# Performance work log

Measured on AMD Instinct MI355X. Metric: run time of the kernel, lower is better.

## Reference

```python
import jax, jax.numpy as jnp
import numpy as np

N_NODES, N_EDGES = 50000, 800000
N_IN, E_IN, N_OUT, E_OUT = 64, 32, 64, 32


def _xavier(key, fan_in, fan_out):
    std = (2.0 / (fan_in + fan_out)) ** 0.5
    return jax.random.normal(key, (fan_in, fan_out), dtype=jnp.float32) * std


def setup_inputs() -> dict:
    key = jax.random.key(0)
    ks = jax.random.split(key, 10)
    return {
        "feat": jax.random.normal(ks[0], (N_NODES, N_IN), dtype=jnp.float32),
        "edge_feat": jax.random.normal(ks[1], (N_EDGES, E_IN), dtype=jnp.float32),
        "w_msg": _xavier(ks[2], N_IN + E_IN, N_OUT),
        "b_msg": jnp.zeros((N_OUT,), dtype=jnp.float32),
        "w_node": _xavier(ks[3], N_IN + N_OUT, N_OUT),
        "b_node": jnp.zeros((N_OUT,), dtype=jnp.float32),
        "w_edge": _xavier(ks[4], N_IN + N_OUT + E_IN, E_OUT),
        "b_edge": jnp.zeros((E_OUT,), dtype=jnp.float32),
        "src_idx": jax.random.randint(ks[5], (N_EDGES,), 0, N_NODES, dtype=jnp.int32),
        "dst_idx": jax.random.randint(ks[6], (N_EDGES,), 0, N_NODES, dtype=jnp.int32),
    }


def reference(feat, edge_feat, w_msg, b_msg, w_node, b_node, w_edge, b_edge, src_idx, dst_idx):
    n_nodes = feat.shape[0]
    # --- message: gather src + edge, linear, tanh --- [E, n_out]
    src_h = feat[src_idx]
    m = jnp.tanh(jnp.concatenate([src_h, edge_feat], axis=1) @ w_msg + b_msg)
    # --- scatter-mean into destination nodes --- [N, n_out]
    sums = jax.ops.segment_sum(m, dst_idx, num_segments=n_nodes)
    cnt = jax.ops.segment_sum(jnp.ones((m.shape[0], 1), m.dtype), dst_idx, num_segments=n_nodes)
    neigh = sums / jnp.maximum(cnt, 1.0)
    # --- node update: cat([neigh, h]) -> linear -> tanh (dropout = identity in eval) ---
    h = jnp.tanh(jnp.concatenate([neigh, feat], axis=1) @ w_node + b_node)
    # --- edge update: cat([src h, dst neigh(updated), edge h]) -> linear -> tanh ---
    e = jnp.tanh(jnp.concatenate([src_h, h[dst_idx], edge_feat], axis=1) @ w_edge + b_edge)
    return h, e
```

## Files before the change

### kernel.cpp

```cpp
#include <hip/hip_runtime.h>

#define NNODES 50000
#define NEDGES 800000
#define NPAD   50176
#define NTILE_E (NEDGES / 16)
#define NTILE_N (NNODES / 16)

typedef __attribute__((ext_vector_type(8))) short bf16x8;
typedef __attribute__((ext_vector_type(4))) float f32x4;

union ABu { bf16x8 v; uint4 u; };

__device__ __forceinline__ float fast_tanh(float x) {
    float e = __expf(2.0f * x);
    return 1.0f - 2.0f * __builtin_amdgcn_rcpf(e + 1.0f);
}

__device__ __forceinline__ unsigned pk_rne(float x, float y) {
    unsigned a = __float_as_uint(x), b = __float_as_uint(y);
    a = (a + 0x7fffu + ((a >> 16) & 1u)) >> 16;
    b = (b + 0x7fffu + ((b >> 16) & 1u)) >> 16;
    return a | (b << 16);
}
__device__ __forceinline__ unsigned pk_tr(float a, float b) {
    return __builtin_amdgcn_perm(__float_as_uint(b), __float_as_uint(a), 0x07060302);
}
__device__ __forceinline__ float bf16_lo(unsigned u) { return __uint_as_float(u << 16); }
__device__ __forceinline__ float bf16_hi(unsigned u) { return __uint_as_float(u & 0xffff0000u); }

__device__ __forceinline__ ABu make_afrag(const float* p) {
    float4 a = ((const float4*)p)[0];
    float4 b = ((const float4*)p)[1];
    ABu r;
    r.u.x = pk_tr(a.x, a.y); r.u.y = pk_tr(a.z, a.w);
    r.u.z = pk_tr(b.x, b.y); r.u.w = pk_tr(b.z, b.w);
    return r;
}

template <int LDN>
__device__ __forceinline__ ABu make_bfrag_u(const unsigned* wp) {
    ABu r;
    r.u.x = wp[0 * LDN]; r.u.y = wp[1 * LDN];
    r.u.z = wp[2 * LDN]; r.u.w = wp[3 * LDN];
    return r;
}

template <int KH, int N>
__device__ __forceinline__ void stage_w(const float* __restrict__ w, unsigned* wl_u) {
    for (int i = threadIdx.x; i < KH * N; i += 256) {
        const int kp = i / N, n = i % N;
        wl_u[i] = pk_rne(w[(2 * kp) * N + n], w[(2 * kp + 1) * N + n]);
    }
}

#define MFMA(a, b, c) __builtin_amdgcn_mfma_f32_16x16x32_bf16((a).v, (b).v, (c), 0, 0, 0)

__global__ __launch_bounds__(256) void hist_kernel(const int* __restrict__ dst_idx,
                                                   int* __restrict__ cnt,
                                                   int* __restrict__ rank) {
    const int base = (blockIdx.x * 256 + threadIdx.x) * 4;
    if (base + 4 <= NEDGES) {
        int4 d = *(const int4*)(dst_idx + base);
        int4 r;
        r.x = atomicAdd(&cnt[d.x], 1);
        r.y = atomicAdd(&cnt[d.y], 1);
        r.z = atomicAdd(&cnt[d.z], 1);
        r.w = atomicAdd(&cnt[d.w], 1);
        *(int4*)(rank + base) = r;
    } else {
        for (int i = base; i < NEDGES; ++i) rank[i] = atomicAdd(&cnt[dst_idx[i]], 1);
    }
}

__global__ __launch_bounds__(256) void scan1(const int* __restrict__ cnt,
                                             int* __restrict__ off,
                                             int* __restrict__ btot) {
    __shared__ int s[256];
    const int tid = threadIdx.x;
    const int g = blockIdx.x * 256 + tid;
    const int own = cnt[g];
    s[tid] = own;
    __syncthreads();
    for (int o = 1; o < 256; o <<= 1) {
        int v = (tid >= o) ? s[tid - o] : 0;
        __syncthreads();
        s[tid] += v;
        __syncthreads();
    }
    off[g] = s[tid] - own;
    if (tid == 255) btot[blockIdx.x] = s[255];
}

__global__ __launch_bounds__(256) void scan2(int* __restrict__ btot) {
    __shared__ int s[256];
    const int tid = threadIdx.x;
    const int own = btot[tid];
    s[tid] = own;
    __syncthreads();
    for (int o = 1; o < 256; o <<= 1) {
        int v = (tid >= o) ? s[tid - o] : 0;
        __syncthreads();
        s[tid] += v;
        __syncthreads();
    }
    btot[tid] = s[tid] - own;
}

__global__ __launch_bounds__(256) void scan3(int* __restrict__ off,
                                             const int* __restrict__ btot) {
    const int g = blockIdx.x * 256 + threadIdx.x;
    off[g] += btot[blockIdx.x];
}

struct MsgBuf { ABu a0, a1, a2; int4 rows; };

__device__ __forceinline__ void msg_load(
    int t, int col, int quad,
    const float* __restrict__ feat, const float* __restrict__ edge_feat,
    const int* __restrict__ src_idx, const int* __restrict__ dst_idx,
    const int* __restrict__ off, const int* __restrict__ rank, MsgBuf& b) {
    const int e0 = t << 4;
    const int e = e0 + col;
    const int src = src_idx[e];
    const int4 d4 = *(const int4*)(dst_idx + e0 + (quad << 2));
    const int4 r4 = *(const int4*)(rank + e0 + (quad << 2));
    b.rows.x = off[d4.x] + r4.x;
    b.rows.y = off[d4.y] + r4.y;
    b.rows.z = off[d4.z] + r4.z;
    b.rows.w = off[d4.w] + r4.w;
    b.a0 = make_afrag(feat + (size_t)src * 64 + (quad << 3));
    b.a1 = make_afrag(feat + (size_t)src * 64 + 32 + (quad << 3));
    b.a2 = make_afrag(edge_feat + (size_t)e * 32 + (quad << 3));
}

__device__ __forceinline__ void msg_comp(
    int col, const ABu (&bf)[3][4], const float (&bias)[4],
    const MsgBuf& b, unsigned* __restrict__ m_out) {
    f32x4 acc[4];
#pragma unroll
    for (int nt = 0; nt < 4; ++nt)
        acc[nt] = (f32x4){bias[nt], bias[nt], bias[nt], bias[nt]};
#pragma unroll
    for (int nt = 0; nt < 4; ++nt) {
        acc[nt] = MFMA(b.a0, bf[0][nt], acc[nt]);
        acc[nt] = MFMA(b.a1, bf[1][nt], acc[nt]);
        acc[nt] = MFMA(b.a2, bf[2][nt], acc[nt]);
    }
    const int rw[4] = {b.rows.x, b.rows.y, b.rows.z, b.rows.w};
#pragma unroll
    for (int i = 0; i < 4; ++i) {
        uint2 o;
        o.x = pk_rne(fast_tanh(acc[0][i]), fast_tanh(acc[1][i]));
        o.y = pk_rne(fast_tanh(acc[2][i]), fast_tanh(acc[3][i]));
        *(uint2*)(m_out + (size_t)rw[i] * 32 + (col << 1)) = o;
    }
}

__global__ __launch_bounds__(256) void msg_kernel(
    const float* __restrict__ feat, const float* __restrict__ edge_feat,
    const float* __restrict__ w_msg, const float* __restrict__ b_msg,
    const int* __restrict__ src_idx, const int* __restrict__ dst_idx,
    const int* __restrict__ off, const int* __restrict__ rank,
    unsigned* __restrict__ m_out) {
    __shared__ __align__(16) unsigned wl[48 * 64];
    stage_w<48, 64>(w_msg, wl);
    __syncthreads();

    const int lane = threadIdx.x & 63, wave = threadIdx.x >> 6;
    const int col = lane & 15, quad = lane >> 4;

    ABu bf[3][4];
#pragma unroll
    for (int kc = 0; kc < 3; ++kc)
#pragma unroll
        for (int nt = 0; nt < 4; ++nt)
            bf[kc][nt] = make_bfrag_u<64>(&wl[(kc * 16 + (quad << 2)) * 64 + nt * 16 + col]);

    float bias[4];
#pragma unroll
    for (int nt = 0; nt < 4; ++nt) bias[nt] = b_msg[nt * 16 + col];

    const int nw = gridDim.x << 2;
    int t = (blockIdx.x << 2) + wave;
    if (t >= NTILE_E) return;
    MsgBuf A, B;
    msg_load(t, col, quad, feat, edge_feat, src_idx, dst_idx, off, rank, A);
    for (;;) {
        const int t2 = t + nw;
        if (t2 < NTILE_E)
            msg_load(t2, col, quad, feat, edge_feat, src_idx, dst_idx, off, rank, B);
        msg_comp(col, bf, bias, A, m_out);
        if (t2 >= NTILE_E) return;
        const int t3 = t2 + nw;
        if (t3 < NTILE_E)
            msg_load(t3, col, quad, feat, edge_feat, src_idx, dst_idx, off, rank, A);
        msg_comp(col, bf, bias, B, m_out);
        if (t3 >= NTILE_E) return;
        t = t3;
    }
}

__global__ __launch_bounds__(256) void gather_kernel(
    const unsigned* __restrict__ m,
    const int* __restrict__ off , const int* __restrict__ cnt,
    float* __restrict__ neigh) {
    const int wave = threadIdx.x >> 6;
    const int lane = threadIdx.x & 63;
    const int n = blockIdx.x * 4 + wave;
    if (n >= NNODES) return;
    const int c = cnt[n];
    const int o = off[n];
    const int q = lane & 7;
    const int g = lane >> 3;

    float s[8];
#pragma unroll
    for (int j = 0; j < 8; ++j) s[j] = 0.f;
    for (int r = g; r < c; r += 8) {
        const uint4 u = *(const uint4*)(m + (size_t)(o + r) * 32 + (q << 2));
        s[0] += bf16_lo(u.x); s[1] += bf16_hi(u.x);
        s[2] += bf16_lo(u.y); s[3] += bf16_hi(u.y);
        s[4] += bf16_lo(u.z); s[5] += bf16_hi(u.z);
        s[6] += bf16_lo(u.w); s[7] += bf16_hi(u.w);
    }
#pragma unroll
    for (int j = 0; j < 8; ++j) {
        s[j] += __shfl_xor(s[j], 8);
        s[j] += __shfl_xor(s[j], 16);
        s[j] += __shfl_xor(s[j], 32);
    }
    if (g == 0) {
        const float inv = __builtin_amdgcn_rcpf((float)max(c, 1));
        float4 o0 = {s[0] * inv, s[1] * inv, s[2] * inv, s[3] * inv};
        float4 o1 = {s[4] * inv, s[5] * inv, s[6] * inv, s[7] * inv};
        float* dst = neigh + (size_t)n * 64 + (q << 3);
        ((float4*)dst)[0] = o0;
        ((float4*)dst)[1] = o1;
    }
}

__device__ __forceinline__ int mapk(int ks) {
    return ks < 64 ? ((ks >> 2) + ((ks >> 1) & 1) * 32 + (ks & 1) * 16) : ks;
}

__global__ __launch_bounds__(256) void node_update(
    const float* __restrict__ feat,
    const float* __restrict__ w_node, const float* __restrict__ b_node,
    float* __restrict__ h) {
    __shared__ __align__(16) float wl[128 * 64];
    for (int i = threadIdx.x; i < 128 * 64; i += 256) wl[i] = w_node[i];
    __syncthreads();

    const int lane = threadIdx.x & 63, wave = threadIdx.x >> 6;
    const int col = lane & 15, quad = lane >> 4;

    ABu bf[4][4];
#pragma unroll
    for (int kc = 0; kc < 4; ++kc)
#pragma unroll
        for (int nt = 0; nt < 4; ++nt) {
            unsigned p[4];
#pragma unroll
            for (int jj = 0; jj < 4; ++jj) {
                const int k0 = kc * 32 + quad * 8 + jj * 2;
                p[jj] = pk_rne(wl[mapk(k0) * 64 + nt * 16 + col],
                               wl[mapk(k0 + 1) * 64 + nt * 16 + col]);
            }
            bf[kc][nt].u = (uint4){p[0], p[1], p[2], p[3]};
        }

    float bias[4];
#pragma unroll
    for (int nt = 0; nt < 4; ++nt) bias[nt] = b_node[nt * 16 + col];

    const int nw = gridDim.x << 2;
    for (int t = (blockIdx.x << 2) + wave; t < NTILE_N; t += nw) {
        const int n0 = t << 4;
        const int n = n0 + col;
        ABu a0 = make_afrag(h + (size_t)n * 64 + quad * 8);
        ABu a1 = make_afrag(h + (size_t)n * 64 + 32 + quad * 8);
        ABu a2 = make_afrag(feat + (size_t)n * 64 + quad * 8);
        ABu a3 = make_afrag(feat + (size_t)n * 64 + 32 + quad * 8);

        f32x4 acc[4];
#pragma unroll
        for (int nt = 0; nt < 4; ++nt)
            acc[nt] = (f32x4){bias[nt], bias[nt], bias[nt], bias[nt]};
#pragma unroll
        for (int nt = 0; nt < 4; ++nt) {
            acc[nt] = MFMA(a0, bf[0][nt], acc[nt]);
            acc[nt] = MFMA(a1, bf[1][nt], acc[nt]);
            acc[nt] = MFMA(a2, bf[2][nt], acc[nt]);
            acc[nt] = MFMA(a3, bf[3][nt], acc[nt]);
        }
#pragma unroll
        for (int i = 0; i < 4; ++i) {
            const int nr = n0 + quad * 4 + i;
#pragma unroll
            for (int nt = 0; nt < 4; ++nt)
                h[(size_t)nr * 64 + nt * 16 + col] = fast_tanh(acc[nt][i]);
        }
    }
}

struct EBuf { ABu a0, a1, a2, a3, a4; };

__device__ __forceinline__ void edge_load(
    int t, int col, int quad,
    const float* __restrict__ feat, const float* __restrict__ edge_feat,
    const float* __restrict__ h,
    const int* __restrict__ src_idx, const int* __restrict__ dst_idx, EBuf& b) {
    const int e = (t << 4) + col;
    const int src = src_idx[e];
    const int dst = dst_idx[e];
    b.a0 = make_afrag(feat + (size_t)src * 64 + (quad << 3));
    b.a1 = make_afrag(feat + (size_t)src * 64 + 32 + (quad << 3));
    b.a2 = make_afrag(h + (size_t)dst * 64 + (quad << 3));
    b.a3 = make_afrag(h + (size_t)dst * 64 + 32 + (quad << 3));
    b.a4 = make_afrag(edge_feat + (size_t)e * 32 + (quad << 3));
}

__device__ __forceinline__ void edge_comp(
    int t, int col, int quad, const ABu (&bf)[5][2], const float (&bias)[2],
    const EBuf& b, float* __restrict__ e_out) {
    f32x4 acc[2];
#pragma unroll
    for (int nt = 0; nt < 2; ++nt)
        acc[nt] = (f32x4){bias[nt], bias[nt], bias[nt], bias[nt]};
#pragma unroll
    for (int nt = 0; nt < 2; ++nt) {
        acc[nt] = MFMA(b.a0, bf[0][nt], acc[nt]);
        acc[nt] = MFMA(b.a1, bf[1][nt], acc[nt]);
        acc[nt] = MFMA(b.a2, bf[2][nt], acc[nt]);
        acc[nt] = MFMA(b.a3, bf[3][nt], acc[nt]);
        acc[nt] = MFMA(b.a4, bf[4][nt], acc[nt]);
    }
    const int e0 = t << 4;
#pragma unroll
    for (int i = 0; i < 4; ++i) {
        const int er = e0 + quad * 4 + i;
        e_out[(size_t)er * 32 + col] = fast_tanh(acc[0][i]);
        e_out[(size_t)er * 32 + 16 + col] = fast_tanh(acc[1][i]);
    }
}

__global__ __launch_bounds__(256) void edge_update(
    const float* __restrict__ feat, const float* __restrict__ edge_feat,
    const float* __restrict__ h,
    const float* __restrict__ w_edge, const float* __restrict__ b_edge,
    const int* __restrict__ src_idx, const int* __restrict__ dst_idx,
    float* __restrict__ e_out) {
    __shared__ __align__(16) unsigned wl[80 * 32];
    stage_w<80, 32>(w_edge, wl);
    __syncthreads();

    const int lane = threadIdx.x & 63, wave = threadIdx.x >> 6;
    const int col = lane & 15, quad = lane >> 4;

    ABu bf[5][2];
#pragma unroll
    for (int kc = 0; kc < 5; ++kc)
#pragma unroll
        for (int nt = 0; nt < 2; ++nt)
            bf[kc][nt] = make_bfrag_u<32>(&wl[(kc * 16 + (quad << 2)) * 32 + nt * 16 + col]);

    float bias[2];
#pragma unroll
    for (int nt = 0; nt < 2; ++nt) bias[nt] = b_edge[nt * 16 + col];

    const int nw = gridDim.x << 2;
    int t = (blockIdx.x << 2) + wave;
    if (t >= NTILE_E) return;
    EBuf A, B;
    edge_load(t, col, quad, feat, edge_feat, h, src_idx, dst_idx, A);
    for (;;) {
        const int t2 = t + nw;
        if (t2 < NTILE_E)
            edge_load(t2, col, quad, feat, edge_feat, h, src_idx, dst_idx, B);
        edge_comp(t, col, quad, bf, bias, A, e_out);
        if (t2 >= NTILE_E) return;
        const int t3 = t2 + nw;
        if (t3 < NTILE_E)
            edge_load(t3, col, quad, feat, edge_feat, h, src_idx, dst_idx, A);
        edge_comp(t2, col, quad, bf, bias, B, e_out);
        if (t3 >= NTILE_E) return;
        t = t3;
    }
}

extern "C" void kernel_launch(void* const* d_in, const int* in_sizes, int n_in,
                              void* d_out, int out_size, void* d_ws, size_t ws_size,
                              hipStream_t stream) {
    const float* feat      = (const float*)d_in[0];
    const float* edge_feat = (const float*)d_in[1];
    const float* w_msg     = (const float*)d_in[2];
    const float* b_msg     = (const float*)d_in[3];
    const float* w_node    = (const float*)d_in[4];
    const float* b_node    = (const float*)d_in[5];
    const float* w_edge    = (const float*)d_in[6];
    const float* b_edge    = (const float*)d_in[7];
    const int*   src_idx   = (const int*)d_in[8];
    const int*   dst_idx   = (const int*)d_in[9];

    float* h = (float*)d_out;
    float* e = (float*)d_out + (size_t)NNODES * 64;
    unsigned* m = (unsigned*)e;

    int* cnt  = (int*)d_ws;
    int* off  = cnt + NPAD;
    int* btot = off + NPAD;
    int* rank = btot + 256;

    hipMemsetAsync(cnt, 0, NPAD * sizeof(int), stream);
    hipMemsetAsync(btot, 0, 256 * sizeof(int), stream);

    hist_kernel<<<(NEDGES / 4 + 255) / 256, 256, 0, stream>>>(dst_idx, cnt, rank);
    scan1<<<NPAD / 256, 256, 0, stream>>>(cnt, off, btot);
    scan2<<<1, 256, 0, stream>>>(btot);
    scan3<<<NPAD / 256, 256, 0, stream>>>(off, btot);
    msg_kernel<<<1536, 256, 0, stream>>>(feat, edge_feat, w_msg, b_msg,
                                         src_idx, dst_idx, off, rank, m);
    gather_kernel<<<NNODES / 4, 256, 0, stream>>>(m, off, cnt, h);
    node_update<<<512, 256, 0, stream>>>(feat, w_node, b_node, h);
    edge_update<<<1280, 256, 0, stream>>>(feat, edge_feat, h, w_edge,
                                          b_edge, src_idx, dst_idx, e);
}
```

Measured before the change: 414.6 us.

## Precompute per-node projections before gathering in message and edge kernels

The message and edge linear layers are split by linearity. The feat and h parts are projected once per node (50K rows) by a new proj_kernel, and the edge kernels then gather the smaller projected rows instead of the raw 64-wide features. This cuts per-edge MFMA work and per-edge gather width: the edge kernel gathers 32+32 floats instead of 128, and the message kernel gathers 64 projected floats. It adds three small projection launches and workspace buffers. The message projection reuses the h output buffer as scratch before the gather kernel writes h.

```diff
diff --git a/kernel.cpp b/kernel.cpp
--- a/kernel.cpp
+++ b/kernel.cpp
@@ -112,89 +112,134 @@
     off[g] += btot[blockIdx.x];
 }
 
-struct MsgBuf { ABu a0, a1, a2; int4 rows; };
+template <int KC, int NT>
+__global__ __launch_bounds__(256) void proj_kernel(
+    const float* __restrict__ in, const float* __restrict__ w,
+    const float* __restrict__ bias, float* __restrict__ out) {
+    constexpr int N = NT * 16;
+    constexpr int K = KC * 32;
+    __shared__ __align__(16) unsigned wl[(K / 2) * N];
+    stage_w<K / 2, N>(w, wl);
+    __syncthreads();
+
+    const int lane = threadIdx.x & 63, wave = threadIdx.x >> 6;
+    const int col = lane & 15, quad = lane >> 4;
+
+    ABu bf[KC][NT];
+#pragma unroll
+    for (int kc = 0; kc < KC; ++kc)
+#pragma unroll
+        for (int nt = 0; nt < NT; ++nt)
+            bf[kc][nt] = make_bfrag_u<N>(&wl[(kc * 16 + (quad << 2)) * N + nt * 16 + col]);
+
+    float bi[NT];
+#pragma unroll
+    for (int nt = 0; nt < NT; ++nt) bi[nt] = bias ? bias[nt * 16 + col] : 0.f;
+
+    const int nw = gridDim.x << 2;
+    for (int t = (blockIdx.x << 2) + wave; t < NTILE_N; t += nw) {
+        const int n0 = t << 4;
+        const int n = n0 + col;
+        ABu a[KC];
+#pragma unroll
+        for (int kc = 0; kc < KC; ++kc)
+            a[kc] = make_afrag(in + (size_t)n * K + kc * 32 + (quad << 3));
+
+        f32x4 acc[NT];
+#pragma unroll
+        for (int nt = 0; nt < NT; ++nt)
+            acc[nt] = (f32x4){bi[nt], bi[nt], bi[nt], bi[nt]};
+#pragma unroll
+        for (int nt = 0; nt < NT; ++nt)
+#pragma unroll
+            for (int kc = 0; kc < KC; ++kc)
+                acc[nt] = MFMA(a[kc], bf[kc][nt], acc[nt]);
+
+#pragma unroll
+        for (int i = 0; i < 4; ++i) {
+            const int nr = n0 + (quad << 2) + i;
+            if (NT == 4) {
+                float4 o = {acc[0][i], acc[1][i], acc[2][i], acc[3][i]};
+                *(float4*)(out + (size_t)nr * 64 + (col << 2)) = o;
+            } else {
+                float2 o = {acc[0][i], acc[1][i]};
+                *(float2*)(out + (size_t)nr * 32 + (col << 1)) = o;
+            }
+        }
+    }
+}
+
+struct MsgBuf { ABu a2; float4 f4[4]; int4 rows; };
 
 __device__ __forceinline__ void msg_load(
     int t, int col, int quad,
-    const float* __restrict__ feat, const float* __restrict__ edge_feat,
+    const float* __restrict__ edge_feat, const float* __restrict__ projm,
     const int* __restrict__ src_idx, const int* __restrict__ dst_idx,
     const int* __restrict__ off, const int* __restrict__ rank, MsgBuf& b) {
     const int e0 = t << 4;
-    const int e = e0 + col;
-    const int src = src_idx[e];
+    const int4 s4 = *(const int4*)(src_idx + e0 + (quad << 2));
     const int4 d4 = *(const int4*)(dst_idx + e0 + (quad << 2));
     const int4 r4 = *(const int4*)(rank + e0 + (quad << 2));
     b.rows.x = off[d4.x] + r4.x;
     b.rows.y = off[d4.y] + r4.y;
     b.rows.z = off[d4.z] + r4.z;
     b.rows.w = off[d4.w] + r4.w;
-    b.a0 = make_afrag(feat + (size_t)src * 64 + (quad << 3));
-    b.a1 = make_afrag(feat + (size_t)src * 64 + 32 + (quad << 3));
-    b.a2 = make_afrag(edge_feat + (size_t)e * 32 + (quad << 3));
+    b.a2 = make_afrag(edge_feat + (size_t)(e0 + col) * 32 + (quad << 3));
+    b.f4[0] = *(const float4*)(projm + (size_t)s4.x * 64 + (col << 2));
+    b.f4[1] = *(const float4*)(projm + (size_t)s4.y * 64 + (col << 2));
+    b.f4[2] = *(const float4*)(projm + (size_t)s4.z * 64 + (col << 2));
+    b.f4[3] = *(const float4*)(projm + (size_t)s4.w * 64 + (col << 2));
 }
 
 __device__ __forceinline__ void msg_comp(
-    int col, const ABu (&bf)[3][4], const float (&bias)[4],
-    const MsgBuf& b, unsigned* __restrict__ m_out) {
+    int col, const ABu (&bf)[4], const MsgBuf& b, unsigned* __restrict__ m_out) {
     f32x4 acc[4];
 #pragma unroll
-    for (int nt = 0; nt < 4; ++nt)
-        acc[nt] = (f32x4){bias[nt], bias[nt], bias[nt], bias[nt]};
-#pragma unroll
-    for (int nt = 0; nt < 4; ++nt) {
-        acc[nt] = MFMA(b.a0, bf[0][nt], acc[nt]);
-        acc[nt] = MFMA(b.a1, bf[1][nt], acc[nt]);
-        acc[nt] = MFMA(b.a2, bf[2][nt], acc[nt]);
-    }
+    for (int nt = 0; nt < 4; ++nt) acc[nt] = (f32x4){0.f, 0.f, 0.f, 0.f};
+#pragma unroll
+    for (int nt = 0; nt < 4; ++nt) acc[nt] = MFMA(b.a2, bf[nt], acc[nt]);
     const int rw[4] = {b.rows.x, b.rows.y, b.rows.z, b.rows.w};
 #pragma unroll
     for (int i = 0; i < 4; ++i) {
         uint2 o;
-        o.x = pk_rne(fast_tanh(acc[0][i]), fast_tanh(acc[1][i]));
-        o.y = pk_rne(fast_tanh(acc[2][i]), fast_tanh(acc[3][i]));
+        o.x = pk_rne(fast_tanh(acc[0][i] + b.f4[i].x), fast_tanh(acc[1][i] + b.f4[i].y));
+        o.y = pk_rne(fast_tanh(acc[2][i] + b.f4[i].z), fast_tanh(acc[3][i] + b.f4[i].w));
         *(uint2*)(m_out + (size_t)rw[i] * 32 + (col << 1)) = o;
     }
 }
 
 __global__ __launch_bounds__(256) void msg_kernel(
-    const float* __restrict__ feat, const float* __restrict__ edge_feat,
-    const float* __restrict__ w_msg, const float* __restrict__ b_msg,
+    const float* __restrict__ edge_feat, const float* __restrict__ w_bot,
     const int* __restrict__ src_idx, const int* __restrict__ dst_idx,
     const int* __restrict__ off, const int* __restrict__ rank,
-    unsigned* __restrict__ m_out) {
-    __shared__ __align__(16) unsigned wl[48 * 64];
-    stage_w<48, 64>(w_msg, wl);
+    const float* __restrict__ projm, unsigned* __restrict__ m_out) {
+    __shared__ __align__(16) unsigned wl[16 * 64];
+    stage_w<16, 64>(w_bot, wl);
     __syncthreads();
 
     const int lane = threadIdx.x & 63, wave = threadIdx.x >> 6;
     const int col = lane & 15, quad = lane >> 4;
 
-    ABu bf[3][4];
-#pragma unroll
-    for (int kc = 0; kc < 3; ++kc)
-#pragma unroll
-        for (int nt = 0; nt < 4; ++nt)
-            bf[kc][nt] = make_bfrag_u<64>(&wl[(kc * 16 + (quad << 2)) * 64 + nt * 16 + col]);
-
-    float bias[4];
-#pragma unroll
-    for (int nt = 0; nt < 4; ++nt) bias[nt] = b_msg[nt * 16 + col];
+    ABu bf[4];
+#pragma unroll
+    for (int nt = 0; nt < 4; ++nt)
+        bf[nt] = make_bfrag_u<64>(&wl[(quad << 2) * 64 + nt * 16 + col]);
 
     const int nw = gridDim.x << 2;
     int t = (blockIdx.x << 2) + wave;
     if (t >= NTILE_E) return;
     MsgBuf A, B;
-    msg_load(t, col, quad, feat, edge_feat, src_idx, dst_idx, off, rank, A);
+    msg_load(t, col, quad, edge_feat, projm, src_idx, dst_idx, off, rank, A);
     for (;;) {
         const int t2 = t + nw;
         if (t2 < NTILE_E)
-            msg_load(t2, col, quad, feat, edge_feat, src_idx, dst_idx, off, rank, B);
-        msg_comp(col, bf, bias, A, m_out);
+            msg_load(t2, col, quad, edge_feat, projm, src_idx, dst_idx, off, rank, B);
+        msg_comp(col, bf, A, m_out);
         if (t2 >= NTILE_E) return;
         const int t3 = t2 + nw;
         if (t3 < NTILE_E)
-            msg_load(t3, col, quad, feat, edge_feat, src_idx, dst_idx, off, rank, A);
-        msg_comp(col, bf, bias, B, m_out);
+            msg_load(t3, col, quad, edge_feat, projm, src_idx, dst_idx, off, rank, A);
+        msg_comp(col, bf, B, m_out);
         if (t3 >= NTILE_E) return;
         t = t3;
     }
@@ -303,86 +348,76 @@
     }
 }
 
-struct EBuf { ABu a0, a1, a2, a3, a4; };
+struct EBuf { ABu a4; float2 g1[4]; float2 g2[4]; };
 
 __device__ __forceinline__ void edge_load(
     int t, int col, int quad,
-    const float* __restrict__ feat, const float* __restrict__ edge_feat,
-    const float* __restrict__ h,
+    const float* __restrict__ edge_feat,
+    const float* __restrict__ p1, const float* __restrict__ p2,
     const int* __restrict__ src_idx, const int* __restrict__ dst_idx, EBuf& b) {
-    const int e = (t << 4) + col;
-    const int src = src_idx[e];
-    const int dst = dst_idx[e];
-    b.a0 = make_afrag(feat + (size_t)src * 64 + (quad << 3));
-    b.a1 = make_afrag(feat + (size_t)src * 64 + 32 + (quad << 3));
-    b.a2 = make_afrag(h + (size_t)dst * 64 + (quad << 3));
-    b.a3 = make_afrag(h + (size_t)dst * 64 + 32 + (quad << 3));
-    b.a4 = make_afrag(edge_feat + (size_t)e * 32 + (quad << 3));
+    const int e0 = t << 4;
+    const int4 s4 = *(const int4*)(src_idx + e0 + (quad << 2));
+    const int4 d4 = *(const int4*)(dst_idx + e0 + (quad << 2));
+    b.a4 = make_afrag(edge_feat + (size_t)(e0 + col) * 32 + (quad << 3));
+    b.g1[0] = *(const float2*)(p1 + (size_t)s4.x * 32 + (col << 1));
+    b.g1[1] = *(const float2*)(p1 + (size_t)s4.y * 32 + (col << 1));
+    b.g1[2] = *(const float2*)(p1 + (size_t)s4.z * 32 + (col << 1));
+    b.g1[3] = *(const float2*)(p1 + (size_t)s4.w * 32 + (col << 1));
+    b.g2[0] = *(const float2*)(p2 + (size_t)d4.x * 32 + (col << 1));
+    b.g2[1] = *(const float2*)(p2 + (size_t)d4.y * 32 + (col << 1));
+    b.g2[2] = *(const float2*)(p2 + (size_t)d4.z * 32 + (col << 1));
+    b.g2[3] = *(const float2*)(p2 + (size_t)d4.w * 32 + (col << 1));
 }
 
 __device__ __forceinline__ void edge_comp(
-    int t, int col, int quad, const ABu (&bf)[5][2], const float (&bias)[2],
+    int t, int col, int quad, const ABu (&bf)[2],
     const EBuf& b, float* __restrict__ e_out) {
     f32x4 acc[2];
 #pragma unroll
-    for (int nt = 0; nt < 2; ++nt)
-        acc[nt] = (f32x4){bias[nt], bias[nt], bias[nt], bias[nt]};
-#pragma unroll
-    for (int nt = 0; nt < 2; ++nt) {
-        acc[nt] = MFMA(b.a0, bf[0][nt], acc[nt]);
-        acc[nt] = MFMA(b.a1, bf[1][nt], acc[nt]);
-        acc[nt] = MFMA(b.a2, bf[2][nt], acc[nt]);
-        acc[nt] = MFMA(b.a3, bf[3][nt], acc[nt]);
-        acc[nt] = MFMA(b.a4, bf[4][nt], acc[nt]);
-    }
+    for (int nt = 0; nt < 2; ++nt) acc[nt] = (f32x4){0.f, 0.f, 0.f, 0.f};
+#pragma unroll
+    for (int nt = 0; nt < 2; ++nt) acc[nt] = MFMA(b.a4, bf[nt], acc[nt]);
     const int e0 = t << 4;
 #pragma unroll
     for (int i = 0; i < 4; ++i) {
-        const int er = e0 + quad * 4 + i;
-        e_out[(size_t)er * 32 + col] = fast_tanh(acc[0][i]);
-        e_out[(size_t)er * 32 + 16 + col] = fast_tanh(acc[1][i]);
+        const int er = e0 + (quad << 2) + i;
+        e_out[(size_t)er * 32 + col] = fast_tanh(acc[0][i] + b.g1[i].x + b.g2[i].x);
+        e_out[(size_t)er * 32 + 16 + col] = fast_tanh(acc[1][i] + b.g1[i].y + b.g2[i].y);
     }
 }
 
 __global__ __launch_bounds__(256) void edge_update(
-    const float* __restrict__ feat, const float* __restrict__ edge_feat,
-    const float* __restrict__ h,
-    const float* __restrict__ w_edge, const float* __restrict__ b_edge,
+    const float* __restrict__ edge_feat, const float* __restrict__ w3,
+    const float* __restrict__ p1, const float* __restrict__ p2,
     const int* __restrict__ src_idx, const int* __restrict__ dst_idx,
     float* __restrict__ e_out) {
-    __shared__ __align__(16) unsigned wl[80 * 32];
-    stage_w<80, 32>(w_edge, wl);
+    __shared__ __align__(16) unsigned wl[16 * 32];
+    stage_w<16, 32>(w3, wl);
     __syncthreads();
 
     const int lane = threadIdx.x & 63, wave = threadIdx.x >> 6;
     const int col = lane & 15, quad = lane >> 4;
 
-    ABu bf[5][2];
-#pragma unroll
-    for (int kc = 0; kc < 5; ++kc)
-#pragma unroll
-        for (int nt = 0; nt < 2; ++nt)
-            bf[kc][nt] = make_bfrag_u<32>(&wl[(kc * 16 + (quad << 2)) * 32 + nt * 16 + col]);
-
-    float bias[2];
-#pragma unroll
-    for (int nt = 0; nt < 2; ++nt) bias[nt] = b_edge[nt * 16 + col];
+    ABu bf[2];
+#pragma unroll
+    for (int nt = 0; nt < 2; ++nt)
+        bf[nt] = make_bfrag_u<32>(&wl[(quad << 2) * 32 + nt * 16 + col]);
 
     const int nw = gridDim.x << 2;
     int t = (blockIdx.x << 2) + wave;
     if (t >= NTILE_E) return;
     EBuf A, B;
-    edge_load(t, col, quad, feat, edge_feat, h, src_idx, dst_idx, A);
+    edge_load(t, col, quad, edge_feat, p1, p2, src_idx, dst_idx, A);
     for (;;) {
         const int t2 = t + nw;
         if (t2 < NTILE_E)
-            edge_load(t2, col, quad, feat, edge_feat, h, src_idx, dst_idx, B);
-        edge_comp(t, col, quad, bf, bias, A, e_out);
+            edge_load(t2, col, quad, edge_feat, p1, p2, src_idx, dst_idx, B);
+        edge_comp(t, col, quad, bf, A, e_out);
         if (t2 >= NTILE_E) return;
         const int t3 = t2 + nw;
         if (t3 < NTILE_E)
-            edge_load(t3, col, quad, feat, edge_feat, h, src_idx, dst_idx, A);
-        edge_comp(t2, col, quad, bf, bias, B, e_out);
+            edge_load(t3, col, quad, edge_feat, p1, p2, src_idx, dst_idx, A);
+        edge_comp(t2, col, quad, bf, B, e_out);
         if (t3 >= NTILE_E) return;
         t = t3;
     }
@@ -405,11 +440,14 @@
     float* h = (float*)d_out;
     float* e = (float*)d_out + (size_t)NNODES * 64;
     unsigned* m = (unsigned*)e;
+    float* projm = h;
 
     int* cnt  = (int*)d_ws;
     int* off  = cnt + NPAD;
     int* btot = off + NPAD;
     int* rank = btot + 256;
+    float* p1 = (float*)(rank + NEDGES);
+    float* p2 = p1 + (size_t)NNODES * 32;
 
     hipMemsetAsync(cnt, 0, NPAD * sizeof(int), stream);
     hipMemsetAsync(btot, 0, 256 * sizeof(int), stream);
@@ -418,10 +456,13 @@
     scan1<<<NPAD / 256, 256, 0, stream>>>(cnt, off, btot);
     scan2<<<1, 256, 0, stream>>>(btot);
     scan3<<<NPAD / 256, 256, 0, stream>>>(off, btot);
-    msg_kernel<<<1536, 256, 0, stream>>>(feat, edge_feat, w_msg, b_msg,
-                                         src_idx, dst_idx, off, rank, m);
+    proj_kernel<2, 4><<<256, 256, 0, stream>>>(feat, w_msg, b_msg, projm);
+    msg_kernel<<<1280, 256, 0, stream>>>(edge_feat, w_msg + 64 * 64,
+                                         src_idx, dst_idx, off, rank, projm, m);
     gather_kernel<<<NNODES / 4, 256, 0, stream>>>(m, off, cnt, h);
     node_update<<<512, 256, 0, stream>>>(feat, w_node, b_node, h);
-    edge_update<<<1280, 256, 0, stream>>>(feat, edge_feat, h, w_edge,
-                                          b_edge, src_idx, dst_idx, e);
-}
+    proj_kernel<2, 2><<<256, 256, 0, stream>>>(feat, w_edge, b_edge, p1);
+    proj_kernel<2, 2><<<256, 256, 0, stream>>>(h, w_edge + 64 * 32, nullptr, p2);
+    edge_update<<<1280, 256, 0, stream>>>(edge_feat, w_edge + 128 * 32,
+                                          p1, p2, src_idx, dst_idx, e);
+}
```

Measured after the change: 390.2 us. 1.06x faster.
